# Kernel tuning notes

Hardware: AMD Instinct MI355X
Metric: run time of the kernel (lower is better)

## Reference

```python
import jax, jax.numpy as jnp
import numpy as np

WS = 7          # window size
NH = 6          # heads
LN_EPS = 1e-5


def _rel_pos_index(ws):
    coords = np.stack(np.meshgrid(np.arange(ws), np.arange(ws), indexing='ij'))  # (2, ws, ws)
    flat = coords.reshape(2, -1)                       # (2, ws*ws)
    rel = flat[:, :, None] - flat[:, None, :]          # (2, N, N)
    rel = rel.transpose(1, 2, 0).copy()
    rel[:, :, 0] += ws - 1
    rel[:, :, 1] += ws - 1
    rel[:, :, 0] *= 2 * ws - 1
    return jnp.asarray(rel.sum(-1).reshape(-1), dtype=jnp.int32)  # (N*N,)


def _layernorm(x, gamma, beta):
    mu = jnp.mean(x, axis=-1, keepdims=True)
    var = jnp.var(x, axis=-1, keepdims=True)
    return (x - mu) * jax.lax.rsqrt(var + LN_EPS) * gamma + beta


def _window_partition(x, ws):
    B, H, W, C = x.shape
    x = x.reshape(B, H // ws, ws, W // ws, ws, C)
    return x.transpose(0, 1, 3, 2, 4, 5).reshape(-1, ws * ws, C)


def _window_reverse(w, ws, H, W, B):
    C = w.shape[-1]
    x = w.reshape(B, H // ws, W // ws, ws, ws, C)
    return x.transpose(0, 1, 3, 2, 4, 5).reshape(B, H, W, C)


def setup_inputs() -> dict:
    key = jax.random.key(0)
    B, H, W, C = 32, 56, 56, 384
    N, hidden = H * W, 1536
    ks = jax.random.split(key, 9)
    s = 0.02
    return {
        'x':      jax.random.normal(ks[0], (B, N, C), jnp.float32),
        'gamma1': jnp.ones((C,), jnp.float32),
        'beta1':  jnp.zeros((C,), jnp.float32),
        'w_qkv':  jax.random.normal(ks[1], (C, 3 * C), jnp.float32) * s,
        'w_proj': jax.random.normal(ks[2], (C, C), jnp.float32) * s,
        'b_proj': jnp.zeros((C,), jnp.float32),
        'rel_bias': jax.random.normal(ks[3], ((2 * WS - 1) ** 2, NH), jnp.float32) * s,
        'gamma2': jnp.ones((C,), jnp.float32),
        'beta2':  jnp.zeros((C,), jnp.float32),
        'w_fc1':  jax.random.normal(ks[4], (C, hidden), jnp.float32) * s,
        'b_fc1':  jnp.zeros((hidden,), jnp.float32),
        'w_dw':   jax.random.normal(ks[5], (hidden, 1, 3, 3), jnp.float32) * s,
        'b_dw':   jnp.zeros((hidden,), jnp.float32),
        'w_fc2':  jax.random.normal(ks[6], (hidden, C), jnp.float32) * s,
        'b_fc2':  jnp.zeros((C,), jnp.float32),
        'H': H,
        'W': W,
    }


def reference(x, gamma1, beta1, w_qkv, w_proj, b_proj, rel_bias,
              gamma2, beta2, w_fc1, b_fc1, w_dw, b_dw, w_fc2, b_fc2, H, W):
    B, N, C = x.shape
    Nw = WS * WS
    hd = C // NH
    scale = hd ** -0.5

    # ---- window attention branch ----
    shortcut = x
    xn = _layernorm(x, gamma1, beta1)
    xw = _window_partition(xn.reshape(B, H, W, C), WS)      # (Bw, Nw, C)
    Bw = xw.shape[0]
    qkv = (xw @ w_qkv).reshape(Bw, Nw, 3, NH, hd)
    q, k, v = [qkv[:, :, i].transpose(0, 2, 1, 3) for i in range(3)]  # (Bw, NH, Nw, hd)
    attn = jnp.einsum('bhnd,bhmd->bhnm', q, k) * scale
    bias = rel_bias[_rel_pos_index(WS)].reshape(Nw, Nw, NH).transpose(2, 0, 1)
    attn = jax.nn.softmax(attn + bias[None], axis=-1)
    out = jnp.einsum('bhnm,bhmd->bhnd', attn, v).transpose(0, 2, 1, 3).reshape(Bw, Nw, C)
    out = out @ w_proj + b_proj
    x = shortcut + _window_reverse(out, WS, H, W, B).reshape(B, N, C)

    # ---- ConvFFN branch ----
    y = _layernorm(x, gamma2, beta2)
    y = y @ w_fc1 + b_fc1                                    # (B, N, hidden)
    hdim = y.shape[-1]
    y2 = y.transpose(0, 2, 1).reshape(B, hdim, H, W)         # NCHW
    y2 = jax.lax.conv_general_dilated(
        y2, w_dw, window_strides=(1, 1), padding='SAME',
        dimension_numbers=('NCHW', 'OIHW', 'NCHW'),
        feature_group_count=hdim) + b_dw[None, :, None, None]
    y = y2.reshape(B, hdim, N).transpose(0, 2, 1)
    y = jax.nn.gelu(y, approximate=False)
    y = y @ w_fc2 + b_fc2
    return x + y
```

## Files before the change

kernel.cpp:

```cpp
#include <hip/hip_runtime.h>
#include <math.h>


typedef __bf16 bf16x8 __attribute__((ext_vector_type(8)));
typedef float f32x4 __attribute__((ext_vector_type(4)));
typedef unsigned short u16x8 __attribute__((ext_vector_type(8)));

__device__ __forceinline__ float b2f(unsigned short u) {
    union { unsigned int i; float f; } x;
    x.i = ((unsigned int)u) << 16;
    return x.f;
}
__device__ __forceinline__ unsigned short f2b(float f) {
    union { float f; unsigned int i; } x;
    x.f = f;
    unsigned int i = x.i;
    return (unsigned short)((i + 0x7fffu + ((i >> 16) & 1u)) >> 16);
}
__device__ __forceinline__ float rd2(const float* pf, const unsigned short* pb,
                                     long i, int f32) {
    return f32 ? pf[i] : b2f(pb[i]);
}
__device__ __forceinline__ int xr_swz(int r) {
    return (r & 3) ^ ((r >> 2) & 3);
}

__global__ void detect_dtype(const unsigned int* __restrict__ gamma1,
                             int* __restrict__ flag)
{
    if (threadIdx.x == 0) flag[0] = (gamma1[0] == 0x3F800000u) ? 1 : 0;
}

__global__ __launch_bounds__(256) void convert_smalls(
    const int* __restrict__ flag,
    const void* g1, const void* b1, const void* bp, const void* g2,
    const void* b2, const void* bf1, const void* wdw, const void* bdw,
    const void* bf2, const void* rb, unsigned short* __restrict__ dst)
{
    int i = blockIdx.x * 256 + threadIdx.x;
    if (i >= 20214) return;
    const int f = flag[0];
    const void* src; long j; int o = i;
    if      (i < 384)   { src = g1;  j = i; }
    else if (i < 768)   { src = b1;  j = i - 384; }
    else if (i < 1152)  { src = bp;  j = i - 768; }
    else if (i < 1536)  { src = g2;  j = i - 1152; }
    else if (i < 1920)  { src = b2;  j = i - 1536; }
    else if (i < 3456)  { src = bf1; j = i - 1920; }
    else if (i < 17280) {
        int d = i - 3456, k = d / 1536, ch = d % 1536;
        src = wdw; j = (long)ch * 9 + k;
    }
    else if (i < 18816) { src = bdw; j = i - 17280; }
    else if (i < 19200) { src = bf2; j = i - 18816; }
    else                { src = rb;  j = i - 19200; }
    float v = f ? ((const float*)src)[j] : b2f(((const unsigned short*)src)[j]);
    dst[o] = f2b(v);
}

__global__ __launch_bounds__(256) void transpose_any(
    const void* __restrict__ in, unsigned short* __restrict__ out,
    int R, int C, const int* __restrict__ flag)
{
    __shared__ unsigned short tile[32][33];
    const int f = flag[0];
    int tx = threadIdx.x & 31, ty = threadIdx.x >> 5;
    int rb = blockIdx.y * 32, cb = blockIdx.x * 32;
#pragma unroll
    for (int i = 0; i < 32; i += 8) {
        int r = rb + ty + i, c = cb + tx;
        if (r < R && c < C)
            tile[ty + i][tx] = f2b(rd2((const float*)in,
                                       (const unsigned short*)in,
                                       (long)r * C + c, f));
    }
    __syncthreads();
#pragma unroll
    for (int i = 0; i < 32; i += 8) {
        int c = cb + ty + i, r = rb + tx;
        if (c < C && r < R) out[(long)c * R + r] = tile[tx][ty + i];
    }
}

__global__ __launch_bounds__(256) void ln_kernel(
    const float* __restrict__ xf, const unsigned short* __restrict__ xb,
    const unsigned short* __restrict__ gamma,
    const unsigned short* __restrict__ beta,
    unsigned short* __restrict__ yout, int T,
    const int* __restrict__ flagp, int force_f32)
{
    int w = blockIdx.x * 4 + (threadIdx.x >> 6);
    int lane = threadIdx.x & 63;
    if (w >= T) return;
    const int f32 = force_f32 ? 1 : flagp[0];
    long base = (long)w * 384;
    float v[6];
    float s = 0.f;
#pragma unroll
    for (int i = 0; i < 6; ++i) {
        v[i] = rd2(xf, xb, base + lane + i * 64, f32);
        s += v[i];
    }
#pragma unroll
    for (int o = 32; o > 0; o >>= 1) s += __shfl_xor(s, o);
    float mu = s * (1.f / 384.f);
    float q = 0.f;
#pragma unroll
    for (int i = 0; i < 6; ++i) { float d = v[i] - mu; q += d * d; }
#pragma unroll
    for (int o = 32; o > 0; o >>= 1) q += __shfl_xor(q, o);
    float rs = rsqrtf(q * (1.f / 384.f) + 1e-5f);
#pragma unroll
    for (int i = 0; i < 6; ++i) {
        int cc = lane + i * 64;
        yout[base + cc] = f2b((v[i] - mu) * rs * b2f(gamma[cc]) + b2f(beta[cc]));
    }
}

template<int EPI, bool OUT_F32_S, bool RES_F32_S>
__global__ __launch_bounds__(512) void gemm_nt(
    const unsigned short* __restrict__ A,
    const unsigned short* __restrict__ BT,
    float* __restrict__ Cf, unsigned short* __restrict__ Cb,
    const unsigned short* __restrict__ bias,
    const float* __restrict__ Rf, const unsigned short* __restrict__ Rb,
    int M, int N, int K,
    const int* __restrict__ rflagp, const int* __restrict__ oflagp)
{
    __shared__ __align__(16) unsigned short ldsA[2][256 * 32];
    __shared__ __align__(16) unsigned short ldsB[2][128 * 32];
    const int tid = threadIdx.x;
    const int lane = tid & 63;
    const int wv = tid >> 6;
    const int waveM = wv >> 1, waveN = wv & 1;
    const long m0 = (long)blockIdx.x * 256;
    const long n0 = (long)blockIdx.y * 128;

    f32x4 acc[4][4] = {};

    const int ca0 = tid, ca1 = 512 + tid, cb0 = tid;
    const int ra0 = ca0 >> 2, qa0 = (ca0 & 3) ^ xr_swz(ra0);
    const int ra1 = ca1 >> 2, qa1 = (ca1 & 3) ^ xr_swz(ra1);
    const int rb0 = cb0 >> 2, qb0 = (cb0 & 3) ^ xr_swz(rb0);
    long am0 = m0 + ra0; if (am0 >= M) am0 = M - 1;
    long am1 = m0 + ra1; if (am1 >= M) am1 = M - 1;
    const unsigned short* a0p = A + am0 * (long)K + qa0 * 8;
    const unsigned short* a1p = A + am1 * (long)K + qa1 * 8;
    const unsigned short* b0p = BT + (n0 + rb0) * (long)K + qb0 * 8;

    const int rq = lane & 15, quad = lane >> 4;
    const int nt = K >> 5;

    auto STAGE = [&](int buf, int kt) {
        __builtin_amdgcn_global_load_lds(
            (const __attribute__((address_space(1))) void*)(a0p + kt),
            (__attribute__((address_space(3))) void*)(&ldsA[buf][ca0 * 8]), 16, 0, 0);
        __builtin_amdgcn_global_load_lds(
            (const __attribute__((address_space(1))) void*)(a1p + kt),
            (__attribute__((address_space(3))) void*)(&ldsA[buf][ca1 * 8]), 16, 0, 0);
        __builtin_amdgcn_global_load_lds(
            (const __attribute__((address_space(1))) void*)(b0p + kt),
            (__attribute__((address_space(3))) void*)(&ldsB[buf][cb0 * 8]), 16, 0, 0);
    };

    STAGE(0, 0);
    if (nt > 1) STAGE(1, 32);

    for (int t = 0; t < nt; ++t) {
        const int cur = t & 1;
        if (t + 1 < nt) asm volatile("s_waitcnt vmcnt(3)" ::: "memory");
        else            asm volatile("s_waitcnt vmcnt(0)" ::: "memory");
        __builtin_amdgcn_s_barrier();

        bf16x8 af[4], bfv[4];
#pragma unroll
        for (int mi = 0; mi < 4; ++mi) {
            int R = waveM * 64 + mi * 16 + rq;
            int ch = R * 4 + (quad ^ xr_swz(R));
            af[mi] = *(const bf16x8*)(&ldsA[cur][ch * 8]);
        }
#pragma unroll
        for (int ni = 0; ni < 4; ++ni) {
            int R = waveN * 64 + ni * 16 + rq;
            int ch = R * 4 + (quad ^ xr_swz(R));
            bfv[ni] = *(const bf16x8*)(&ldsB[cur][ch * 8]);
        }
#pragma unroll
        for (int mi = 0; mi < 4; ++mi)
#pragma unroll
            for (int ni = 0; ni < 4; ++ni)
                acc[mi][ni] = __builtin_amdgcn_mfma_f32_16x16x32_bf16(
                    af[mi], bfv[ni], acc[mi][ni], 0, 0, 0);

        __builtin_amdgcn_s_barrier();
        if (t + 2 < nt) STAGE(cur, (t + 2) * 32);
    }

    const int res_f32 = rflagp ? rflagp[0] : (RES_F32_S ? 1 : 0);
    const int out_f32 = oflagp ? oflagp[0] : (OUT_F32_S ? 1 : 0);

    const int rq4 = (lane >> 4) * 4;
    const int coln = lane & 15;
#pragma unroll
    for (int mi = 0; mi < 4; ++mi) {
#pragma unroll
        for (int ni = 0; ni < 4; ++ni) {
            long col = n0 + waveN * 64 + ni * 16 + coln;
            float bv = (EPI >= 1) ? b2f(bias[col]) : 0.f;
#pragma unroll
            for (int r = 0; r < 4; ++r) {
                long row = m0 + waveM * 64 + mi * 16 + rq4 + r;
                if (row >= M) continue;
                long off = row * (long)N + col;
                float v = acc[mi][ni][r] + bv;
                if (EPI == 2) v += rd2(Rf, Rb, off, res_f32);
                if (out_f32) Cf[off] = v;
                else Cb[off] = f2b(v);
            }
        }
    }
}

__global__ __launch_bounds__(64) void attn_kernel(
    const unsigned short* __restrict__ qkv,
    const unsigned short* __restrict__ rel_bias,
    unsigned short* __restrict__ out)
{
    __shared__ __align__(16) unsigned short k_lds[64 * 72];
    __shared__ __align__(16) unsigned short v_lds[64 * 72];
    __shared__ __align__(16) unsigned short q_lds[64 * 72];

    const int w = blockIdx.x, hh = blockIdx.y;
    const int lane = threadIdx.x;
    const int b = w >> 6, wh = (w >> 3) & 7, ww = w & 7;
    const long base = (long)b * 3136;
    const unsigned short* src = qkv + hh * 64;

#pragma unroll
    for (int it = 0; it < 13; ++it) {
        int idx = it * 64 + lane;
        if (idx < 784) {
            int t = idx >> 4, d4 = (idx & 15) << 2;
            int pi = t / 7, pj = t % 7;
            const unsigned short* gp =
                src + (base + (wh * 7 + pi) * 56 + (ww * 7 + pj)) * 1152 + d4;
            *(ushort4*)(q_lds + t * 72 + d4) = *(const ushort4*)(gp);
            *(ushort4*)(k_lds + t * 72 + d4) = *(const ushort4*)(gp + 384);
        }
    }
    for (int p = 0; p < 49; ++p) {
        int pi = p / 7, pj = p % 7;
        v_lds[lane * 72 + p] =
            src[(base + (wh * 7 + pi) * 56 + (ww * 7 + pj)) * 1152 + 768 + lane];
    }
#pragma unroll
    for (int p = 49; p < 64; ++p) v_lds[lane * 72 + p] = 0;
    __syncthreads();

    const int rq = lane & 15, quad = lane >> 4;

    bf16x8 kf[4][2], qf[4][2];
#pragma unroll
    for (int t4 = 0; t4 < 4; ++t4)
#pragma unroll
        for (int ks = 0; ks < 2; ++ks) {
            kf[t4][ks] = *(const bf16x8*)(k_lds + (t4 * 16 + rq) * 72 + ks * 32 + quad * 8);
            qf[t4][ks] = *(const bf16x8*)(q_lds + (t4 * 16 + rq) * 72 + ks * 32 + quad * 8);
        }
    f32x4 sa[4][4] = {};
#pragma unroll
    for (int ks = 0; ks < 2; ++ks)
#pragma unroll
        for (int mi = 0; mi < 4; ++mi)
#pragma unroll
            for (int ni = 0; ni < 4; ++ni)
                sa[mi][ni] = __builtin_amdgcn_mfma_f32_16x16x32_bf16(
                    kf[mi][ks], qf[ni][ks], sa[mi][ni], 0, 0, 0);

    const int kq = quad * 4;
#pragma unroll
    for (int ni = 0; ni < 4; ++ni) {
        int q = ni * 16 + rq;
        int qc = (q < 49) ? q : 48;
        int yi = qc / 7, xi = qc % 7;
        float mx = -1e30f;
#pragma unroll
        for (int mi = 0; mi < 4; ++mi)
#pragma unroll
            for (int r = 0; r < 4; ++r) {
                int key = mi * 16 + kq + r;
                float s;
                if (key < 49) {
                    int yj = key / 7, xj = key % 7;
                    int idx = (yi - yj + 6) * 13 + (xi - xj + 6);
                    s = 0.125f * sa[mi][ni][r] + b2f(rel_bias[idx * 6 + hh]);
                } else s = -1e30f;
                sa[mi][ni][r] = s;
                mx = fmaxf(mx, s);
            }
        mx = fmaxf(mx, __shfl_xor(mx, 16));
        mx = fmaxf(mx, __shfl_xor(mx, 32));
        float sum = 0.f;
#pragma unroll
        for (int mi = 0; mi < 4; ++mi)
#pragma unroll
            for (int r = 0; r < 4; ++r) {
                float e = __expf(sa[mi][ni][r] - mx);
                sa[mi][ni][r] = e;
                sum += e;
            }
        sum += __shfl_xor(sum, 16);
        sum += __shfl_xor(sum, 32);
        float rinv = 1.f / sum;
#pragma unroll
        for (int mi = 0; mi < 4; ++mi) {
            unsigned int w0 = (unsigned int)f2b(sa[mi][ni][0] * rinv) |
                              ((unsigned int)f2b(sa[mi][ni][1] * rinv) << 16);
            unsigned int w1 = (unsigned int)f2b(sa[mi][ni][2] * rinv) |
                              ((unsigned int)f2b(sa[mi][ni][3] * rinv) << 16);
            *(unsigned int*)(q_lds + q * 72 + mi * 16 + kq)     = w0;
            *(unsigned int*)(q_lds + q * 72 + mi * 16 + kq + 2) = w1;
        }
    }
    __syncthreads();

    f32x4 oa[4][4] = {};
#pragma unroll
    for (int ks = 0; ks < 2; ++ks) {
        bf16x8 pf[4], vf[4];
#pragma unroll
        for (int qt = 0; qt < 4; ++qt)
            pf[qt] = *(const bf16x8*)(q_lds + (qt * 16 + rq) * 72 + ks * 32 + quad * 8);
#pragma unroll
        for (int dt = 0; dt < 4; ++dt)
            vf[dt] = *(const bf16x8*)(v_lds + (dt * 16 + rq) * 72 + ks * 32 + quad * 8);
#pragma unroll
        for (int qt = 0; qt < 4; ++qt)
#pragma unroll
            for (int dt = 0; dt < 4; ++dt)
                oa[qt][dt] = __builtin_amdgcn_mfma_f32_16x16x32_bf16(
                    pf[qt], vf[dt], oa[qt][dt], 0, 0, 0);
    }

#pragma unroll
    for (int qt = 0; qt < 4; ++qt)
#pragma unroll
        for (int r = 0; r < 4; ++r) {
            int q = qt * 16 + quad * 4 + r;
            if (q >= 49) continue;
            int yi = q / 7, xi = q % 7;
            long t = base + (long)(wh * 7 + yi) * 56 + (ww * 7 + xi);
            unsigned short* op = out + t * 384 + hh * 64;
#pragma unroll
            for (int dt = 0; dt < 4; ++dt)
                op[dt * 16 + rq] = f2b(oa[qt][dt][r]);
        }
}

__global__ __launch_bounds__(192) void dwconv_gelu(
    const unsigned short* __restrict__ h,
    const unsigned short* __restrict__ w_dwT,
    const unsigned short* __restrict__ b_dw,
    unsigned short* __restrict__ g)
{
    const long t = blockIdx.x;
    const int bb = (int)(t / 3136), n = (int)(t % 3136);
    const int r = n / 56, c = n % 56;
    const int ch = threadIdx.x * 8;

    float a[8];
    u16x8 bv = *(const u16x8*)(b_dw + ch);
#pragma unroll
    for (int i = 0; i < 8; ++i) a[i] = b2f(bv[i]);

#pragma unroll
    for (int dr = -1; dr <= 1; ++dr) {
        int rr = r + dr;
        if (rr < 0 || rr >= 56) continue;
#pragma unroll
        for (int dc = -1; dc <= 1; ++dc) {
            int cc = c + dc;
            if (cc < 0 || cc >= 56) continue;
            int k = (dr + 1) * 3 + (dc + 1);
            long off = ((long)bb * 3136 + rr * 56 + cc) * 1536 + ch;
            u16x8 hv = *(const u16x8*)(h + off);
            u16x8 wv = *(const u16x8*)(w_dwT + k * 1536 + ch);
#pragma unroll
            for (int i = 0; i < 8; ++i) a[i] += b2f(hv[i]) * b2f(wv[i]);
        }
    }
    u16x8 ov;
#pragma unroll
    for (int i = 0; i < 8; ++i) {
        float v = 0.5f * a[i] * (1.f + erff(a[i] * 0.70710678118654752f));
        ov[i] = f2b(v);
    }
    *(u16x8*)(g + t * 1536 + ch) = ov;
}

extern "C" void kernel_launch(void* const* d_in, const int* in_sizes, int n_in,
                              void* d_out, int out_size, void* d_ws, size_t ws_size,
                              hipStream_t stream)
{
    const void* x      = d_in[0];
    const void* gamma1 = d_in[1];
    const void* beta1  = d_in[2];
    const void* w_qkv  = d_in[3];
    const void* w_proj = d_in[4];
    const void* b_proj = d_in[5];
    const void* relb   = d_in[6];
    const void* gamma2 = d_in[7];
    const void* beta2  = d_in[8];
    const void* w_fc1  = d_in[9];
    const void* b_fc1  = d_in[10];
    const void* w_dw   = d_in[11];
    const void* b_dw   = d_in[12];
    const void* w_fc2  = d_in[13];
    const void* b_fc2  = d_in[14];

    const int NIMG = 32, NPI = 3136;

    int* flag = (int*)d_ws;
    unsigned short* smalls = (unsigned short*)((char*)d_ws + 16);
    unsigned short* wqkvT  = (unsigned short*)((char*)d_ws + 16 + 20224 * 2);
    unsigned short* wprojT = wqkvT + 1152 * 384;
    unsigned short* wfc1T  = wprojT + 384 * 384;
    unsigned short* wfc2T  = wfc1T + 1536 * 384;
    const size_t WB = 16 + 20224 * 2 +
        ((size_t)1152 * 384 + 384 * 384 + 1536 * 384 + 384 * 1536) * 2;
    char* chunk_base = (char*)d_ws + WB;

    const unsigned short* c_g1   = smalls;
    const unsigned short* c_b1   = smalls + 384;
    const unsigned short* c_bp   = smalls + 768;
    const unsigned short* c_g2   = smalls + 1152;
    const unsigned short* c_b2   = smalls + 1536;
    const unsigned short* c_bf1  = smalls + 1920;
    const unsigned short* c_wdwT = smalls + 3456;
    const unsigned short* c_bdw  = smalls + 17280;
    const unsigned short* c_bf2  = smalls + 18816;
    const unsigned short* c_rb   = smalls + 19200;

    const size_t PER_IMG = (size_t)NPI * 384 * 4 + 2 * (size_t)NPI * 1536 * 2;
    int ipc = NIMG;
    while (ipc > 1 && WB + PER_IMG * (size_t)ipc > ws_size) ipc >>= 1;

    detect_dtype<<<1, 64, 0, stream>>>((const unsigned int*)gamma1, flag);
    convert_smalls<<<80, 256, 0, stream>>>(flag, gamma1, beta1, b_proj, gamma2,
        beta2, b_fc1, w_dw, b_dw, b_fc2, relb, smalls);
    transpose_any<<<dim3(36, 12), 256, 0, stream>>>(w_qkv, wqkvT, 384, 1152, flag);
    transpose_any<<<dim3(12, 12), 256, 0, stream>>>(w_proj, wprojT, 384, 384, flag);
    transpose_any<<<dim3(48, 12), 256, 0, stream>>>(w_fc1, wfc1T, 384, 1536, flag);
    transpose_any<<<dim3(12, 48), 256, 0, stream>>>(w_fc2, wfc2T, 1536, 384, flag);

    for (int i0 = 0; i0 < NIMG; i0 += ipc) {
        const int Tc = ipc * NPI;
        const long tb = (long)i0 * NPI;
        const int GM = (Tc + 255) / 256;

        float* x1 = (float*)chunk_base;
        unsigned short* r1 = (unsigned short*)(chunk_base + (size_t)Tc * 384 * 4);
        unsigned short* r2 = r1 + (size_t)Tc * 1536;

        unsigned short* xn      = r1;
        unsigned short* hbuf    = r1;
        unsigned short* qkv     = r2;
        unsigned short* attnout = r2 + (size_t)Tc * 1152;
        unsigned short* ybuf    = r2;
        unsigned short* gbuf    = r2;

        const float* xf = (const float*)x + tb * 384;
        const unsigned short* xb = (const unsigned short*)x + tb * 384;
        float* of = (float*)d_out + tb * 384;
        unsigned short* ob = (unsigned short*)d_out + tb * 384;

        ln_kernel<<<Tc / 4, 256, 0, stream>>>(xf, xb, c_g1, c_b1, xn, Tc, flag, 0);
        gemm_nt<0, false, false><<<dim3(GM, 9), 512, 0, stream>>>(
            xn, wqkvT, nullptr, qkv, nullptr, nullptr, nullptr,
            Tc, 1152, 384, nullptr, nullptr);
        attn_kernel<<<dim3(ipc * 64, 6), 64, 0, stream>>>(qkv, c_rb, attnout);
        gemm_nt<2, true, false><<<dim3(GM, 3), 512, 0, stream>>>(
            attnout, wprojT, x1, nullptr, c_bp, xf, xb,
            Tc, 384, 384, flag, nullptr);

        ln_kernel<<<Tc / 4, 256, 0, stream>>>(x1, nullptr, c_g2, c_b2, ybuf, Tc,
                                              flag, 1);
        gemm_nt<1, false, false><<<dim3(GM, 12), 512, 0, stream>>>(
            ybuf, wfc1T, nullptr, hbuf, c_bf1, nullptr, nullptr,
            Tc, 1536, 384, nullptr, nullptr);
        dwconv_gelu<<<Tc, 192, 0, stream>>>(hbuf, c_wdwT, c_bdw, gbuf);
        gemm_nt<2, false, true><<<dim3(GM, 3), 512, 0, stream>>>(
            gbuf, wfc2T, of, ob, c_bf2, x1, nullptr,
            Tc, 384, 1536, nullptr, flag);
    }
}
```

Measured before the change: 2.128 ms.

## Deepen GEMM pipeline to triple-buffered K=64 tiles with XCD-aware block remap

Reworks the bf16 MFMA GEMM so each k-step stages a 64-wide K tile into three rotating LDS buffers instead of two 32-wide buffers, with a new 8-way XOR swizzle. The inner loop is split into four interleaved LDS-load/MFMA phases bracketed by barriers and s_setprio. The grid becomes 1D, and block ids are remapped so consecutive tiles land on the same XCD for L2 reuse. This aims to hide global-load latency and cut barrier overhead per FLOP. It raises LDS use to roughly 144KB per block, which limits occupancy to one block per CU and adds extra barriers.

New measurement: 2.138 ms. No clear change (+0.5%).

```diff
diff --git a/kernel.cpp b/kernel.cpp
--- a/kernel.cpp
+++ b/kernel.cpp
@@ -20,9 +20,6 @@
 __device__ __forceinline__ float rd2(const float* pf, const unsigned short* pb,
                                      long i, int f32) {
     return f32 ? pf[i] : b2f(pb[i]);
-}
-__device__ __forceinline__ int xr_swz(int r) {
-    return (r & 3) ^ ((r >> 2) & 3);
 }
 
 __global__ void detect_dtype(const unsigned int* __restrict__ gamma1,
@@ -127,73 +124,135 @@
     int M, int N, int K,
     const int* __restrict__ rflagp, const int* __restrict__ oflagp)
 {
-    __shared__ __align__(16) unsigned short ldsA[2][256 * 32];
-    __shared__ __align__(16) unsigned short ldsB[2][128 * 32];
+    __shared__ __align__(16) unsigned short ldsA[3][256 * 64];
+    __shared__ __align__(16) unsigned short ldsB[3][128 * 64];
     const int tid = threadIdx.x;
     const int lane = tid & 63;
     const int wv = tid >> 6;
     const int waveM = wv >> 1, waveN = wv & 1;
-    const long m0 = (long)blockIdx.x * 256;
-    const long n0 = (long)blockIdx.y * 128;
+
+    const int nwg = (int)gridDim.x;
+    const int orig = (int)blockIdx.x;
+    const int qq = nwg >> 3, rr = nwg & 7, xcd = orig & 7;
+    const int wgid = (xcd < rr ? xcd * (qq + 1)
+                               : rr * (qq + 1) + (xcd - rr) * qq) + (orig >> 3);
+    const int NB = N >> 7;
+    const long m0 = (long)(wgid / NB) * 256;
+    const long n0 = (long)(wgid % NB) * 128;
 
     f32x4 acc[4][4] = {};
 
-    const int ca0 = tid, ca1 = 512 + tid, cb0 = tid;
-    const int ra0 = ca0 >> 2, qa0 = (ca0 & 3) ^ xr_swz(ra0);
-    const int ra1 = ca1 >> 2, qa1 = (ca1 & 3) ^ xr_swz(ra1);
-    const int rb0 = cb0 >> 2, qb0 = (cb0 & 3) ^ xr_swz(rb0);
-    long am0 = m0 + ra0; if (am0 >= M) am0 = M - 1;
-    long am1 = m0 + ra1; if (am1 >= M) am1 = M - 1;
-    const unsigned short* a0p = A + am0 * (long)K + qa0 * 8;
-    const unsigned short* a1p = A + am1 * (long)K + qa1 * 8;
-    const unsigned short* b0p = BT + (n0 + rb0) * (long)K + qb0 * 8;
+    const unsigned short* aptr[4];
+    const unsigned short* bptr[2];
+#pragma unroll
+    for (int i = 0; i < 4; ++i) {
+        int c = tid + i * 512, r = c >> 3, q = (c & 7) ^ (r & 7);
+        long row = m0 + r; if (row >= M) row = M - 1;
+        aptr[i] = A + row * (long)K + q * 8;
+    }
+#pragma unroll
+    for (int i = 0; i < 2; ++i) {
+        int c = tid + i * 512, r = c >> 3, q = (c & 7) ^ (r & 7);
+        bptr[i] = BT + (n0 + r) * (long)K + q * 8;
+    }
+
+    auto STAGE = [&](int buf, int kt) {
+#pragma unroll
+        for (int i = 0; i < 4; ++i)
+            __builtin_amdgcn_global_load_lds(
+                (const __attribute__((address_space(1))) void*)(aptr[i] + kt),
+                (__attribute__((address_space(3))) void*)
+                    (&ldsA[buf][(tid + i * 512) * 8]), 16, 0, 0);
+#pragma unroll
+        for (int i = 0; i < 2; ++i)
+            __builtin_amdgcn_global_load_lds(
+                (const __attribute__((address_space(1))) void*)(bptr[i] + kt),
+                (__attribute__((address_space(3))) void*)
+                    (&ldsB[buf][(tid + i * 512) * 8]), 16, 0, 0);
+    };
+
+    const int nt = K >> 6;
+    STAGE(0, 0);
+    if (nt > 1) STAGE(1, 64);
+    if (nt > 2) STAGE(2, 128);
 
     const int rq = lane & 15, quad = lane >> 4;
-    const int nt = K >> 5;
-
-    auto STAGE = [&](int buf, int kt) {
-        __builtin_amdgcn_global_load_lds(
-            (const __attribute__((address_space(1))) void*)(a0p + kt),
-            (__attribute__((address_space(3))) void*)(&ldsA[buf][ca0 * 8]), 16, 0, 0);
-        __builtin_amdgcn_global_load_lds(
-            (const __attribute__((address_space(1))) void*)(a1p + kt),
-            (__attribute__((address_space(3))) void*)(&ldsA[buf][ca1 * 8]), 16, 0, 0);
-        __builtin_amdgcn_global_load_lds(
-            (const __attribute__((address_space(1))) void*)(b0p + kt),
-            (__attribute__((address_space(3))) void*)(&ldsB[buf][cb0 * 8]), 16, 0, 0);
-    };
-
-    STAGE(0, 0);
-    if (nt > 1) STAGE(1, 32);
 
     for (int t = 0; t < nt; ++t) {
-        const int cur = t & 1;
-        if (t + 1 < nt) asm volatile("s_waitcnt vmcnt(3)" ::: "memory");
-        else            asm volatile("s_waitcnt vmcnt(0)" ::: "memory");
+        const int cur = t % 3;
+        const unsigned short* As = ldsA[cur];
+        const unsigned short* Bs = ldsB[cur];
+
+        const int rem = nt - 1 - t;
+        if (rem >= 2)      asm volatile("s_waitcnt vmcnt(12)" ::: "memory");
+        else if (rem == 1) asm volatile("s_waitcnt vmcnt(6)" ::: "memory");
+        else               asm volatile("s_waitcnt vmcnt(0)" ::: "memory");
         __builtin_amdgcn_s_barrier();
 
-        bf16x8 af[4], bfv[4];
-#pragma unroll
-        for (int mi = 0; mi < 4; ++mi) {
+        auto LDA = [&](int mi, int h) {
             int R = waveM * 64 + mi * 16 + rq;
-            int ch = R * 4 + (quad ^ xr_swz(R));
-            af[mi] = *(const bf16x8*)(&ldsA[cur][ch * 8]);
-        }
-#pragma unroll
-        for (int ni = 0; ni < 4; ++ni) {
+            int ch = R * 8 + ((h * 4 + quad) ^ (R & 7));
+            return *(const bf16x8*)(As + ch * 8);
+        };
+        auto LDB = [&](int ni, int h) {
             int R = waveN * 64 + ni * 16 + rq;
-            int ch = R * 4 + (quad ^ xr_swz(R));
-            bfv[ni] = *(const bf16x8*)(&ldsB[cur][ch * 8]);
-        }
-#pragma unroll
-        for (int mi = 0; mi < 4; ++mi)
-#pragma unroll
-            for (int ni = 0; ni < 4; ++ni)
-                acc[mi][ni] = __builtin_amdgcn_mfma_f32_16x16x32_bf16(
-                    af[mi], bfv[ni], acc[mi][ni], 0, 0, 0);
-
+            int ch = R * 8 + ((h * 4 + quad) ^ (R & 7));
+            return *(const bf16x8*)(Bs + ch * 8);
+        };
+
+        bf16x8 b0, b1, b2, b3, a0, a1;
+        b0 = LDB(0, 0); b1 = LDB(1, 0); b2 = LDB(2, 0); b3 = LDB(3, 0);
+        a0 = LDA(0, 0); a1 = LDA(1, 0);
+        __builtin_amdgcn_s_setprio(1);
+        acc[0][0] = __builtin_amdgcn_mfma_f32_16x16x32_bf16(a0, b0, acc[0][0], 0, 0, 0);
+        acc[0][1] = __builtin_amdgcn_mfma_f32_16x16x32_bf16(a0, b1, acc[0][1], 0, 0, 0);
+        acc[0][2] = __builtin_amdgcn_mfma_f32_16x16x32_bf16(a0, b2, acc[0][2], 0, 0, 0);
+        acc[0][3] = __builtin_amdgcn_mfma_f32_16x16x32_bf16(a0, b3, acc[0][3], 0, 0, 0);
+        acc[1][0] = __builtin_amdgcn_mfma_f32_16x16x32_bf16(a1, b0, acc[1][0], 0, 0, 0);
+        acc[1][1] = __builtin_amdgcn_mfma_f32_16x16x32_bf16(a1, b1, acc[1][1], 0, 0, 0);
+        acc[1][2] = __builtin_amdgcn_mfma_f32_16x16x32_bf16(a1, b2, acc[1][2], 0, 0, 0);
+        acc[1][3] = __builtin_amdgcn_mfma_f32_16x16x32_bf16(a1, b3, acc[1][3], 0, 0, 0);
+        __builtin_amdgcn_s_setprio(0);
         __builtin_amdgcn_s_barrier();
-        if (t + 2 < nt) STAGE(cur, (t + 2) * 32);
+        a0 = LDA(2, 0); a1 = LDA(3, 0);
+        __builtin_amdgcn_s_setprio(1);
+        acc[2][0] = __builtin_amdgcn_mfma_f32_16x16x32_bf16(a0, b0, acc[2][0], 0, 0, 0);
+        acc[2][1] = __builtin_amdgcn_mfma_f32_16x16x32_bf16(a0, b1, acc[2][1], 0, 0, 0);
+        acc[2][2] = __builtin_amdgcn_mfma_f32_16x16x32_bf16(a0, b2, acc[2][2], 0, 0, 0);
+        acc[2][3] = __builtin_amdgcn_mfma_f32_16x16x32_bf16(a0, b3, acc[2][3], 0, 0, 0);
+        acc[3][0] = __builtin_amdgcn_mfma_f32_16x16x32_bf16(a1, b0, acc[3][0], 0, 0, 0);
+        acc[3][1] = __builtin_amdgcn_mfma_f32_16x16x32_bf16(a1, b1, acc[3][1], 0, 0, 0);
+        acc[3][2] = __builtin_amdgcn_mfma_f32_16x16x32_bf16(a1, b2, acc[3][2], 0, 0, 0);
+        acc[3][3] = __builtin_amdgcn_mfma_f32_16x16x32_bf16(a1, b3, acc[3][3], 0, 0, 0);
+        __builtin_amdgcn_s_setprio(0);
+        __builtin_amdgcn_s_barrier();
+        b0 = LDB(0, 1); b1 = LDB(1, 1); b2 = LDB(2, 1); b3 = LDB(3, 1);
+        a0 = LDA(0, 1); a1 = LDA(1, 1);
+        __builtin_amdgcn_s_setprio(1);
+        acc[0][0] = __builtin_amdgcn_mfma_f32_16x16x32_bf16(a0, b0, acc[0][0], 0, 0, 0);
+        acc[0][1] = __builtin_amdgcn_mfma_f32_16x16x32_bf16(a0, b1, acc[0][1], 0, 0, 0);
+        acc[0][2] = __builtin_amdgcn_mfma_f32_16x16x32_bf16(a0, b2, acc[0][2], 0, 0, 0);
+        acc[0][3] = __builtin_amdgcn_mfma_f32_16x16x32_bf16(a0, b3, acc[0][3], 0, 0, 0);
+        acc[1][0] = __builtin_amdgcn_mfma_f32_16x16x32_bf16(a1, b0, acc[1][0], 0, 0, 0);
+        acc[1][1] = __builtin_amdgcn_mfma_f32_16x16x32_bf16(a1, b1, acc[1][1], 0, 0, 0);
+        acc[1][2] = __builtin_amdgcn_mfma_f32_16x16x32_bf16(a1, b2, acc[1][2], 0, 0, 0);
+        acc[1][3] = __builtin_amdgcn_mfma_f32_16x16x32_bf16(a1, b3, acc[1][3], 0, 0, 0);
+        __builtin_amdgcn_s_setprio(0);
+        __builtin_amdgcn_s_barrier();
+        a0 = LDA(2, 1); a1 = LDA(3, 1);
+        __builtin_amdgcn_s_setprio(1);
+        acc[2][0] = __builtin_amdgcn_mfma_f32_16x16x32_bf16(a0, b0, acc[2][0], 0, 0, 0);
+        acc[2][1] = __builtin_amdgcn_mfma_f32_16x16x32_bf16(a0, b1, acc[2][1], 0, 0, 0);
+        acc[2][2] = __builtin_amdgcn_mfma_f32_16x16x32_bf16(a0, b2, acc[2][2], 0, 0, 0);
+        acc[2][3] = __builtin_amdgcn_mfma_f32_16x16x32_bf16(a0, b3, acc[2][3], 0, 0, 0);
+        acc[3][0] = __builtin_amdgcn_mfma_f32_16x16x32_bf16(a1, b0, acc[3][0], 0, 0, 0);
+        acc[3][1] = __builtin_amdgcn_mfma_f32_16x16x32_bf16(a1, b1, acc[3][1], 0, 0, 0);
+        acc[3][2] = __builtin_amdgcn_mfma_f32_16x16x32_bf16(a1, b2, acc[3][2], 0, 0, 0);
+        acc[3][3] = __builtin_amdgcn_mfma_f32_16x16x32_bf16(a1, b3, acc[3][3], 0, 0, 0);
+        __builtin_amdgcn_s_setprio(0);
+
+        __builtin_amdgcn_s_barrier();
+        if (t + 3 < nt) STAGE(cur, (t + 3) * 64);
     }
 
     const int res_f32 = rflagp ? rflagp[0] : (RES_F32_S ? 1 : 0);
@@ -475,21 +534,21 @@
         unsigned short* ob = (unsigned short*)d_out + tb * 384;
 
         ln_kernel<<<Tc / 4, 256, 0, stream>>>(xf, xb, c_g1, c_b1, xn, Tc, flag, 0);
-        gemm_nt<0, false, false><<<dim3(GM, 9), 512, 0, stream>>>(
+        gemm_nt<0, false, false><<<GM * 9, 512, 0, stream>>>(
             xn, wqkvT, nullptr, qkv, nullptr, nullptr, nullptr,
             Tc, 1152, 384, nullptr, nullptr);
         attn_kernel<<<dim3(ipc * 64, 6), 64, 0, stream>>>(qkv, c_rb, attnout);
-        gemm_nt<2, true, false><<<dim3(GM, 3), 512, 0, stream>>>(
+        gemm_nt<2, true, false><<<GM * 3, 512, 0, stream>>>(
             attnout, wprojT, x1, nullptr, c_bp, xf, xb,
             Tc, 384, 384, flag, nullptr);
 
         ln_kernel<<<Tc / 4, 256, 0, stream>>>(x1, nullptr, c_g2, c_b2, ybuf, Tc,
                                               flag, 1);
-        gemm_nt<1, false, false><<<dim3(GM, 12), 512, 0, stream>>>(
+        gemm_nt<1, false, false><<<GM * 12, 512, 0, stream>>>(
             ybuf, wfc1T, nullptr, hbuf, c_bf1, nullptr, nullptr,
             Tc, 1536, 384, nullptr, nullptr);
         dwconv_gelu<<<Tc, 192, 0, stream>>>(hbuf, c_wdwT, c_bdw, gbuf);
-        gemm_nt<2, false, true><<<dim3(GM, 3), 512, 0, stream>>>(
+        gemm_nt<2, false, true><<<GM * 3, 512, 0, stream>>>(
             gbuf, wfc2T, of, ob, c_bf2, x1, nullptr,
             Tc, 384, 1536, nullptr, flag);
     }
```
